# Kernel optimization log

Measured on AMD Instinct MI355X. Metric: run time of the kernel, lower is better.

Reference implementation:

```python
import jax, jax.numpy as jnp
import numpy as np

EPS = 1e-5  # torch LayerNorm default

def _layernorm(x, g, b):
    m = x.mean(-1, keepdims=True)
    v = ((x - m) ** 2).mean(-1, keepdims=True)
    return (x - m) * jax.lax.rsqrt(v + EPS) * g + b

def setup_inputs() -> dict:
    key = jax.random.key(0)
    ks = jax.random.split(key, 6)
    B, T, D, N, L = 16, 4096, 512, 77, 768
    s = 0.02
    return {
        "x": jax.random.normal(ks[0], (B, T, D), jnp.float32),
        "xf": jax.random.normal(ks[1], (B, N, L), jnp.float32),
        "q_w": jax.random.normal(ks[2], (D, D), jnp.float32) * s,
        "q_b": jnp.zeros((D,), jnp.float32),
        "k_w": jax.random.normal(ks[3], (D, L), jnp.float32) * s,
        "k_b": jnp.zeros((D,), jnp.float32),
        "v_w": jax.random.normal(ks[4], (D, L), jnp.float32) * s,
        "v_b": jnp.zeros((D,), jnp.float32),
        "norm_g": jnp.ones((D,), jnp.float32),
        "norm_b": jnp.zeros((D,), jnp.float32),
        "tnorm_g": jnp.ones((L,), jnp.float32),
        "tnorm_b": jnp.zeros((L,), jnp.float32),
        "num_heads": 8,
    }

def reference(x, xf, q_w, q_b, k_w, k_b, v_w, v_b, norm_g, norm_b, tnorm_g, tnorm_b, num_heads):
    B, T, D = x.shape
    N = xf.shape[1]
    H = num_heads
    xn = _layernorm(x, norm_g, norm_b)          # [B,T,D]
    xfn = _layernorm(xf, tnorm_g, tnorm_b)      # [B,N,L]
    # projections (torch Linear: y = x @ W^T + b)
    q = (xn @ q_w.T + q_b).reshape(B, T, H, -1)
    k = (xfn @ k_w.T + k_b).reshape(B, N, H, -1)
    v = (xfn @ v_w.T + v_b).reshape(B, N, H, -1)
    q = jax.nn.softmax(q, axis=-1)              # softmax over head feature dim
    k = jax.nn.softmax(k, axis=1)               # softmax over text token dim N
    # context: per-head [d,l] matrix, never materializes T x N scores
    att = jnp.einsum('bnhd,bnhl->bhdl', k, v)   # [B,H,d,l]
    y = jnp.einsum('bthd,bhdl->bthl', q, att).reshape(B, T, D)
    return x + y
```

## Files before the change

kernel.cpp:

```cpp
#include <hip/hip_runtime.h>

typedef __attribute__((ext_vector_type(8))) __bf16 bf16x8;
typedef __attribute__((ext_vector_type(4))) float f32x4;
typedef __attribute__((ext_vector_type(8))) unsigned short u16x8;
typedef __attribute__((ext_vector_type(4))) unsigned short u16x4;

#define MFMA16(a, b, c) __builtin_amdgcn_mfma_f32_16x16x32_bf16((a), (b), (c), 0, 0, 0)

static __device__ __forceinline__ unsigned short f2bf(float f) {
    union { float f; unsigned int u; } v;
    v.f = f;
    unsigned int r = v.u + 0x7FFFu + ((v.u >> 16) & 1u);
    return (unsigned short)(r >> 16);
}

__global__ __launch_bounds__(256) void prep_kernel(
    const float* __restrict__ qw, const float* __restrict__ kw,
    const float* __restrict__ vw,
    unsigned short* __restrict__ wfrag, unsigned short* __restrict__ kv_wf)
{
    const int idx = blockIdx.x * 256 + threadIdx.x;
    if (idx < 262144) {
        const int i = idx & 7, lane = (idx >> 3) & 63, kk = (idx >> 9) & 15, nb = idx >> 13;
        const int row = nb * 16 + (lane & 15);
        const int col = kk * 32 + ((lane >> 4) << 3) + i;
        wfrag[idx] = f2bf(qw[row * 512 + col]);
    } else {
        const int jdx = idx - 262144;
        const int i = jdx & 7, lane = (jdx >> 3) & 63;
        const int rest = jdx >> 9;
        const int kk = rest % 24, nb = rest / 24;
        const int j = nb * 16 + (lane & 15);
        const int k = kk * 32 + ((lane >> 4) << 3) + i;
        kv_wf[jdx] = f2bf(j < 512 ? kw[j * 768 + k] : vw[(j - 512) * 768 + k]);
    }
}

#define LDK 776
__global__ __launch_bounds__(256) void kv_kernel(
    const float* __restrict__ xf, const unsigned short* __restrict__ kv_wf,
    const float* __restrict__ kb, const float* __restrict__ vb,
    const float* __restrict__ tg, const float* __restrict__ tb,
    float* __restrict__ kv)
{
    __shared__ unsigned short xfn[80 * LDK];
    const int tid = threadIdx.x;
    const int lane = tid & 63;
    const int w = tid >> 6;
    const int l15 = lane & 15;
    const int lg = lane >> 4;
    const int b = blockIdx.y;
    const int jt = blockIdx.x;

    float g[12], be[12];
#pragma unroll
    for (int c = 0; c < 3; ++c) {
        const float4 gv = *(const float4*)(tg + c * 256 + lane * 4);
        const float4 bv = *(const float4*)(tb + c * 256 + lane * 4);
        g[c*4+0]=gv.x; g[c*4+1]=gv.y; g[c*4+2]=gv.z; g[c*4+3]=gv.w;
        be[c*4+0]=bv.x; be[c*4+1]=bv.y; be[c*4+2]=bv.z; be[c*4+3]=bv.w;
    }

    for (int n = w; n < 77; n += 4) {
        const float* xr = xf + (long)(b * 77 + n) * 768;
        float vals[12];
#pragma unroll
        for (int c = 0; c < 3; ++c) {
            const float4 v4 = *(const float4*)(xr + c * 256 + lane * 4);
            vals[c*4+0]=v4.x; vals[c*4+1]=v4.y; vals[c*4+2]=v4.z; vals[c*4+3]=v4.w;
        }
        float s = 0.f, ss = 0.f;
#pragma unroll
        for (int j = 0; j < 12; ++j) { s += vals[j]; ss += vals[j] * vals[j]; }
#pragma unroll
        for (int off = 32; off > 0; off >>= 1) {
            s += __shfl_xor(s, off);
            ss += __shfl_xor(ss, off);
        }
        const float mean = s * (1.f / 768.f);
        const float var = ss * (1.f / 768.f) - mean * mean;
        const float rstd = rsqrtf(var + 1e-5f);
#pragma unroll
        for (int c = 0; c < 3; ++c) {
            u16x4 o;
#pragma unroll
            for (int q = 0; q < 4; ++q)
                o[q] = f2bf((vals[c*4+q] - mean) * rstd * g[c*4+q] + be[c*4+q]);
            *(u16x4*)&xfn[n * LDK + c * 256 + lane * 4] = o;
        }
    }
    for (int idx = tid; idx < 3 * 768; idx += 256)
        xfn[(77 + idx / 768) * LDK + (idx % 768)] = 0;
    __syncthreads();

    const int nb = jt * 4 + w;
    f32x4 acc[5];
#pragma unroll
    for (int m = 0; m < 5; ++m) { acc[m][0]=0.f; acc[m][1]=0.f; acc[m][2]=0.f; acc[m][3]=0.f; }
    for (int kk = 0; kk < 24; ++kk) {
        const bf16x8 bw = *(const bf16x8*)&kv_wf[((nb * 24 + kk) * 64 + lane) * 8];
#pragma unroll
        for (int m = 0; m < 5; ++m) {
            const bf16x8 a = *(const bf16x8*)&xfn[(m * 16 + l15) * LDK + kk * 32 + lg * 8];
            acc[m] = MFMA16(a, bw, acc[m]);
        }
    }
    const int j = nb * 16 + l15;
    const float bias = (j < 512) ? kb[j] : vb[j - 512];
#pragma unroll
    for (int m = 0; m < 5; ++m) {
#pragma unroll
        for (int reg = 0; reg < 4; ++reg) {
            const int n = m * 16 + lg * 4 + reg;
            if (n < 77)
                kv[(long)(b * 77 + n) * 1024 + j] = acc[m][reg] + bias;
        }
    }
}

__global__ __launch_bounds__(256) void att_kernel(
    const float* __restrict__ kv, unsigned short* __restrict__ att_fr)
{
    const int b = blockIdx.x >> 3;
    const int h = blockIdx.x & 7;
    __shared__ float k_lds[77][65];
    __shared__ float v_lds[77][65];
    __shared__ float att_lds[64][65];
    const int tid = threadIdx.x;

    for (int idx = tid; idx < 77 * 64; idx += 256) {
        const int n = idx >> 6, d = idx & 63;
        const long base = (long)(b * 77 + n) * 1024 + h * 64 + d;
        k_lds[n][d] = kv[base];
        v_lds[n][d] = kv[base + 512];
    }
    __syncthreads();
    if (tid < 64) {
        float mx = -1e30f;
        for (int n = 0; n < 77; ++n) mx = fmaxf(mx, k_lds[n][tid]);
        float s = 0.f;
        for (int n = 0; n < 77; ++n) {
            const float e = __expf(k_lds[n][tid] - mx);
            k_lds[n][tid] = e;
            s += e;
        }
        const float inv = 1.f / s;
        for (int n = 0; n < 77; ++n) k_lds[n][tid] *= inv;
    }
    __syncthreads();
    {
        const int l = tid & 63, db = (tid >> 6) * 16;
        float a[16];
#pragma unroll
        for (int i = 0; i < 16; ++i) a[i] = 0.f;
        for (int n = 0; n < 77; ++n) {
            const float vv = v_lds[n][l];
#pragma unroll
            for (int i = 0; i < 16; ++i) a[i] += k_lds[n][db + i] * vv;
        }
#pragma unroll
        for (int i = 0; i < 16; ++i) att_lds[db + i][l] = a[i];
    }
    __syncthreads();
    const long hb8 = (long)(b * 8 + h) * 4096;
    for (int idx = tid; idx < 4096; idx += 256) {
        const int i = idx & 7, lane = (idx >> 3) & 63, kk = (idx >> 9) & 1, nf = (idx >> 10);
        const int d = kk * 32 + ((lane >> 4) << 3) + i;
        const int l = nf * 16 + (lane & 15);
        att_fr[hb8 + (long)(nf * 2 + kk) * 512 + lane * 8 + i] = f2bf(att_lds[d][l]);
    }
}

#define LDA 520
#define LDY 516

#define WLD(n, kk) (*(const bf16x8*)&wfrag[((((wc * 8 + (n)) * 16 + (kk)) * 64) + lane) * 8])
#define ALD(m, kk) (*(const bf16x8*)&xn[(wr * 32 + (m) * 16 + l15) * LDA + (kk) * 32 + lg * 8])

__global__ __launch_bounds__(512, 4) void fused3(
    const float* __restrict__ x, const unsigned short* __restrict__ wfrag,
    const float* __restrict__ qb, const float* __restrict__ ng,
    const float* __restrict__ nbt, const unsigned short* __restrict__ att_fr,
    float* __restrict__ out)
{
    __shared__ char smem[64 * LDA * 2];
    unsigned short* const xn = (unsigned short*)smem;
    float* const ylds = (float*)smem;
    const int tid = threadIdx.x;
    const int lane = tid & 63;
    const int w = tid >> 6;
    const int l15 = lane & 15;
    const int lg = lane >> 4;
    const int wr = w >> 2, wc = w & 3;
    const int b = blockIdx.y;
    const long rowbase = (long)b * 4096 + (long)blockIdx.x * 64;
    const float* xblk = x + rowbase * 512;

    float g[8], be[8];
    {
        const float4 g0 = *(const float4*)(ng + lane * 8);
        const float4 g1 = *(const float4*)(ng + lane * 8 + 4);
        const float4 b0 = *(const float4*)(nbt + lane * 8);
        const float4 b1 = *(const float4*)(nbt + lane * 8 + 4);
        g[0]=g0.x; g[1]=g0.y; g[2]=g0.z; g[3]=g0.w;
        g[4]=g1.x; g[5]=g1.y; g[6]=g1.z; g[7]=g1.w;
        be[0]=b0.x; be[1]=b0.y; be[2]=b0.z; be[3]=b0.w;
        be[4]=b1.x; be[5]=b1.y; be[6]=b1.z; be[7]=b1.w;
    }

    {
        float vals[8][8];
#pragma unroll
        for (int r = 0; r < 8; ++r) {
            const float* xr = xblk + (w * 8 + r) * 512 + lane * 8;
            const float4 v0 = *(const float4*)xr;
            const float4 v1 = *(const float4*)(xr + 4);
            vals[r][0]=v0.x; vals[r][1]=v0.y; vals[r][2]=v0.z; vals[r][3]=v0.w;
            vals[r][4]=v1.x; vals[r][5]=v1.y; vals[r][6]=v1.z; vals[r][7]=v1.w;
        }
#pragma unroll
        for (int r = 0; r < 8; ++r) {
            float s = 0.f, ss = 0.f;
#pragma unroll
            for (int j = 0; j < 8; ++j) { s += vals[r][j]; ss += vals[r][j] * vals[r][j]; }
#pragma unroll
            for (int off = 32; off > 0; off >>= 1) {
                s += __shfl_xor(s, off);
                ss += __shfl_xor(ss, off);
            }
            const float mean = s * (1.f / 512.f);
            const float var = ss * (1.f / 512.f) - mean * mean;
            const float rstd = rsqrtf(var + 1e-5f);
            u16x8 o;
#pragma unroll
            for (int j = 0; j < 8; ++j)
                o[j] = f2bf((vals[r][j] - mean) * rstd * g[j] + be[j]);
            *(u16x8*)&xn[(w * 8 + r) * LDA + lane * 8] = o;
        }
    }
    __syncthreads();

    const int wcol = wc * 128;
    f32x4 acc[2][8];
#pragma unroll
    for (int n = 0; n < 8; ++n) {
        const float qbv = qb[wcol + n * 16 + l15];
#pragma unroll
        for (int m = 0; m < 2; ++m) {
            acc[m][n][0]=qbv; acc[m][n][1]=qbv; acc[m][n][2]=qbv; acc[m][n][3]=qbv;
        }
    }

    bf16x8 aC0 = ALD(0, 0), aC1 = ALD(1, 0);
    bf16x8 bC0 = WLD(0, 0), bC1 = WLD(1, 0), bC2 = WLD(2, 0), bC3 = WLD(3, 0);
#pragma unroll
    for (int kk = 0; kk < 16; ++kk) {
        bf16x8 bN0 = WLD(4, kk), bN1 = WLD(5, kk), bN2 = WLD(6, kk), bN3 = WLD(7, kk);
        acc[0][0] = MFMA16(aC0, bC0, acc[0][0]); acc[1][0] = MFMA16(aC1, bC0, acc[1][0]);
        acc[0][1] = MFMA16(aC0, bC1, acc[0][1]); acc[1][1] = MFMA16(aC1, bC1, acc[1][1]);
        acc[0][2] = MFMA16(aC0, bC2, acc[0][2]); acc[1][2] = MFMA16(aC1, bC2, acc[1][2]);
        acc[0][3] = MFMA16(aC0, bC3, acc[0][3]); acc[1][3] = MFMA16(aC1, bC3, acc[1][3]);
        bf16x8 a2_0 = aC0, a2_1 = aC1;
        if (kk < 15) {
            a2_0 = ALD(0, kk + 1); a2_1 = ALD(1, kk + 1);
            bC0 = WLD(0, kk + 1); bC1 = WLD(1, kk + 1);
            bC2 = WLD(2, kk + 1); bC3 = WLD(3, kk + 1);
        }
        acc[0][4] = MFMA16(aC0, bN0, acc[0][4]); acc[1][4] = MFMA16(aC1, bN0, acc[1][4]);
        acc[0][5] = MFMA16(aC0, bN1, acc[0][5]); acc[1][5] = MFMA16(aC1, bN1, acc[1][5]);
        acc[0][6] = MFMA16(aC0, bN2, acc[0][6]); acc[1][6] = MFMA16(aC1, bN2, acc[1][6]);
        acc[0][7] = MFMA16(aC0, bN3, acc[0][7]); acc[1][7] = MFMA16(aC1, bN3, acc[1][7]);
        aC0 = a2_0; aC1 = a2_1;
    }

#pragma unroll
    for (int m = 0; m < 2; ++m) {
#pragma unroll
        for (int hb = 0; hb < 2; ++hb) {
#pragma unroll
            for (int reg = 0; reg < 4; ++reg) {
                float mx = fmaxf(fmaxf(acc[m][hb*4+0][reg], acc[m][hb*4+1][reg]),
                                 fmaxf(acc[m][hb*4+2][reg], acc[m][hb*4+3][reg]));
#pragma unroll
                for (int off = 1; off < 16; off <<= 1)
                    mx = fmaxf(mx, __shfl_xor(mx, off));
                const float e0 = __expf(acc[m][hb*4+0][reg] - mx);
                const float e1 = __expf(acc[m][hb*4+1][reg] - mx);
                const float e2 = __expf(acc[m][hb*4+2][reg] - mx);
                const float e3 = __expf(acc[m][hb*4+3][reg] - mx);
                float sm = e0 + e1 + e2 + e3;
#pragma unroll
                for (int off = 1; off < 16; off <<= 1)
                    sm += __shfl_xor(sm, off);
                const float inv = 1.f / sm;
                acc[m][hb*4+0][reg] = e0 * inv;
                acc[m][hb*4+1][reg] = e1 * inv;
                acc[m][hb*4+2][reg] = e2 * inv;
                acc[m][hb*4+3][reg] = e3 * inv;
            }
        }
    }

    const int h = w;
    const int colbase = h * 64;
    bf16x8 att_b[2][4];
#pragma unroll
    for (int kk = 0; kk < 2; ++kk)
#pragma unroll
        for (int nf = 0; nf < 4; ++nf)
            att_b[kk][nf] = *(const bf16x8*)&att_fr[
                (long)(b * 8 + h) * 4096 + (long)(nf * 2 + kk) * 512 + lane * 8];

    __syncthreads();
#pragma unroll
    for (int m = 0; m < 2; ++m)
#pragma unroll
        for (int n = 0; n < 8; ++n)
#pragma unroll
            for (int reg = 0; reg < 4; ++reg)
                xn[(wr * 32 + m * 16 + lg * 4 + reg) * LDA + wcol + n * 16 + l15] =
                    f2bf(acc[m][n][reg]);
    __syncthreads();

    f32x4 acc2[4][4];
#pragma unroll
    for (int m2 = 0; m2 < 4; ++m2)
#pragma unroll
        for (int nf = 0; nf < 4; ++nf) {
            acc2[m2][nf][0]=0.f; acc2[m2][nf][1]=0.f; acc2[m2][nf][2]=0.f; acc2[m2][nf][3]=0.f;
        }
#pragma unroll
    for (int kk = 0; kk < 2; ++kk) {
        bf16x8 a2[4];
#pragma unroll
        for (int m2 = 0; m2 < 4; ++m2)
            a2[m2] = *(const bf16x8*)&xn[(m2 * 16 + l15) * LDA + colbase + kk * 32 + lg * 8];
#pragma unroll
        for (int nf = 0; nf < 4; ++nf) {
#pragma unroll
            for (int m2 = 0; m2 < 4; ++m2)
                acc2[m2][nf] = MFMA16(a2[m2], att_b[kk][nf], acc2[m2][nf]);
        }
    }
    __syncthreads();

#pragma unroll
    for (int hh = 0; hh < 2; ++hh) {
#pragma unroll
        for (int m2h = 0; m2h < 2; ++m2h) {
            const int m2 = hh * 2 + m2h;
#pragma unroll
            for (int nf = 0; nf < 4; ++nf)
#pragma unroll
                for (int reg = 0; reg < 4; ++reg)
                    ylds[(m2h * 16 + lg * 4 + reg) * LDY + colbase + nf * 16 + l15] =
                        acc2[m2][nf][reg];
        }
        __syncthreads();
        const int row = tid >> 4;
        const long grow = rowbase + hh * 32 + row;
#pragma unroll
        for (int j = 0; j < 8; ++j) {
            const int col = j * 64 + (tid & 15) * 4;
            const float4 yv = *(const float4*)&ylds[row * LDY + col];
            const long gi = grow * 512 + col;
            const float4 xv = *(const float4*)&x[gi];
            float4 ov;
            ov.x = xv.x + yv.x; ov.y = xv.y + yv.y;
            ov.z = xv.z + yv.z; ov.w = xv.w + yv.w;
            *(float4*)&out[gi] = ov;
        }
        __syncthreads();
    }
}

extern "C" void kernel_launch(void* const* d_in, const int* in_sizes, int n_in,
                              void* d_out, int out_size, void* d_ws, size_t ws_size,
                              hipStream_t stream) {
    const float* x  = (const float*)d_in[0];
    const float* xf = (const float*)d_in[1];
    const float* qw = (const float*)d_in[2];
    const float* qb = (const float*)d_in[3];
    const float* kw = (const float*)d_in[4];
    const float* kb = (const float*)d_in[5];
    const float* vw = (const float*)d_in[6];
    const float* vb = (const float*)d_in[7];
    const float* ng = (const float*)d_in[8];
    const float* nb = (const float*)d_in[9];
    const float* tg = (const float*)d_in[10];
    const float* tb = (const float*)d_in[11];
    float* out = (float*)d_out;

    char* ws = (char*)d_ws;
    unsigned short* wfrag  = (unsigned short*)(ws);
    unsigned short* kv_wf  = (unsigned short*)(ws + 524288);
    float*          kv     = (float*)(ws + 2097152);
    unsigned short* att_fr = (unsigned short*)(ws + 7143424);

    prep_kernel<<<dim3(4096), dim3(256), 0, stream>>>(qw, kw, vw, wfrag, kv_wf);
    kv_kernel<<<dim3(16, 16), dim3(256), 0, stream>>>(xf, kv_wf, kb, vb, tg, tb, kv);
    att_kernel<<<dim3(128), dim3(256), 0, stream>>>(kv, att_fr);
    fused3<<<dim3(64, 16), dim3(512), 0, stream>>>(x, wfrag, qb, ng, nb, att_fr, out);
}
```

Before: 156.5 us.

## Assign each wave one head's full 64x64 Q tile to drop a barrier

The Q-projection GEMM is re-tiled so that each of the 8 waves computes all 64 rows for its own 64-column head slice, replacing the earlier 32x128 per-wave tile. The head-feature softmax and the following context matmul then stay within one wave. The barrier between writing bf16 Q to LDS and reading it back can be removed because each wave only reads the columns it wrote. The trade-off is that each wave now loads 4 A fragments and 4 B fragments per k-step instead of 2 and 8, and the per-step software prefetch pattern changes.

```diff
diff --git a/kernel.cpp b/kernel.cpp
--- a/kernel.cpp
+++ b/kernel.cpp
@@ -174,10 +174,10 @@
 #define LDA 520
 #define LDY 516
 
-#define WLD(n, kk) (*(const bf16x8*)&wfrag[((((wc * 8 + (n)) * 16 + (kk)) * 64) + lane) * 8])
-#define ALD(m, kk) (*(const bf16x8*)&xn[(wr * 32 + (m) * 16 + l15) * LDA + (kk) * 32 + lg * 8])
-
-__global__ __launch_bounds__(512, 4) void fused3(
+#define WLD(n, kk) (*(const bf16x8*)&wfrag[((((w * 4 + (n)) * 16 + (kk)) * 64) + lane) * 8])
+#define ALD(m, kk) (*(const bf16x8*)&xn[((m) * 16 + l15) * LDA + (kk) * 32 + lg * 8])
+
+__global__ __launch_bounds__(512, 4) void fused4(
     const float* __restrict__ x, const unsigned short* __restrict__ wfrag,
     const float* __restrict__ qb, const float* __restrict__ ng,
     const float* __restrict__ nbt, const unsigned short* __restrict__ att_fr,
@@ -191,7 +191,6 @@
     const int w = tid >> 6;
     const int l15 = lane & 15;
     const int lg = lane >> 4;
-    const int wr = w >> 2, wc = w & 3;
     const int b = blockIdx.y;
     const long rowbase = (long)b * 4096 + (long)blockIdx.x * 64;
     const float* xblk = x + rowbase * 512;
@@ -240,87 +239,89 @@
     }
     __syncthreads();
 
-    const int wcol = wc * 128;
-    f32x4 acc[2][8];
-#pragma unroll
-    for (int n = 0; n < 8; ++n) {
+    const int wcol = w * 64;
+    f32x4 acc[4][4];
+#pragma unroll
+    for (int n = 0; n < 4; ++n) {
         const float qbv = qb[wcol + n * 16 + l15];
 #pragma unroll
-        for (int m = 0; m < 2; ++m) {
+        for (int m = 0; m < 4; ++m) {
             acc[m][n][0]=qbv; acc[m][n][1]=qbv; acc[m][n][2]=qbv; acc[m][n][3]=qbv;
         }
     }
 
-    bf16x8 aC0 = ALD(0, 0), aC1 = ALD(1, 0);
-    bf16x8 bC0 = WLD(0, 0), bC1 = WLD(1, 0), bC2 = WLD(2, 0), bC3 = WLD(3, 0);
-#pragma unroll
-    for (int kk = 0; kk < 16; ++kk) {
-        bf16x8 bN0 = WLD(4, kk), bN1 = WLD(5, kk), bN2 = WLD(6, kk), bN3 = WLD(7, kk);
-        acc[0][0] = MFMA16(aC0, bC0, acc[0][0]); acc[1][0] = MFMA16(aC1, bC0, acc[1][0]);
-        acc[0][1] = MFMA16(aC0, bC1, acc[0][1]); acc[1][1] = MFMA16(aC1, bC1, acc[1][1]);
-        acc[0][2] = MFMA16(aC0, bC2, acc[0][2]); acc[1][2] = MFMA16(aC1, bC2, acc[1][2]);
-        acc[0][3] = MFMA16(aC0, bC3, acc[0][3]); acc[1][3] = MFMA16(aC1, bC3, acc[1][3]);
-        bf16x8 a2_0 = aC0, a2_1 = aC1;
-        if (kk < 15) {
-            a2_0 = ALD(0, kk + 1); a2_1 = ALD(1, kk + 1);
-            bC0 = WLD(0, kk + 1); bC1 = WLD(1, kk + 1);
-            bC2 = WLD(2, kk + 1); bC3 = WLD(3, kk + 1);
-        }
-        acc[0][4] = MFMA16(aC0, bN0, acc[0][4]); acc[1][4] = MFMA16(aC1, bN0, acc[1][4]);
-        acc[0][5] = MFMA16(aC0, bN1, acc[0][5]); acc[1][5] = MFMA16(aC1, bN1, acc[1][5]);
-        acc[0][6] = MFMA16(aC0, bN2, acc[0][6]); acc[1][6] = MFMA16(aC1, bN2, acc[1][6]);
-        acc[0][7] = MFMA16(aC0, bN3, acc[0][7]); acc[1][7] = MFMA16(aC1, bN3, acc[1][7]);
-        aC0 = a2_0; aC1 = a2_1;
-    }
-
-#pragma unroll
-    for (int m = 0; m < 2; ++m) {
-#pragma unroll
-        for (int hb = 0; hb < 2; ++hb) {
-#pragma unroll
-            for (int reg = 0; reg < 4; ++reg) {
-                float mx = fmaxf(fmaxf(acc[m][hb*4+0][reg], acc[m][hb*4+1][reg]),
-                                 fmaxf(acc[m][hb*4+2][reg], acc[m][hb*4+3][reg]));
-#pragma unroll
-                for (int off = 1; off < 16; off <<= 1)
-                    mx = fmaxf(mx, __shfl_xor(mx, off));
-                const float e0 = __expf(acc[m][hb*4+0][reg] - mx);
-                const float e1 = __expf(acc[m][hb*4+1][reg] - mx);
-                const float e2 = __expf(acc[m][hb*4+2][reg] - mx);
-                const float e3 = __expf(acc[m][hb*4+3][reg] - mx);
-                float sm = e0 + e1 + e2 + e3;
-#pragma unroll
-                for (int off = 1; off < 16; off <<= 1)
-                    sm += __shfl_xor(sm, off);
-                const float inv = 1.f / sm;
-                acc[m][hb*4+0][reg] = e0 * inv;
-                acc[m][hb*4+1][reg] = e1 * inv;
-                acc[m][hb*4+2][reg] = e2 * inv;
-                acc[m][hb*4+3][reg] = e3 * inv;
+    {
+        bf16x8 aC[4], bC[4];
+#pragma unroll
+        for (int m = 0; m < 4; ++m) aC[m] = ALD(m, 0);
+#pragma unroll
+        for (int n = 0; n < 4; ++n) bC[n] = WLD(n, 0);
+#pragma unroll
+        for (int kk = 0; kk < 16; ++kk) {
+            bf16x8 aN[4], bN[4];
+            if (kk < 15) {
+#pragma unroll
+                for (int m = 0; m < 4; ++m) aN[m] = ALD(m, kk + 1);
+#pragma unroll
+                for (int n = 0; n < 4; ++n) bN[n] = WLD(n, kk + 1);
             }
-        }
-    }
-
-    const int h = w;
-    const int colbase = h * 64;
+#pragma unroll
+            for (int n = 0; n < 4; ++n)
+#pragma unroll
+                for (int m = 0; m < 4; ++m)
+                    acc[m][n] = MFMA16(aC[m], bC[n], acc[m][n]);
+            if (kk < 15) {
+#pragma unroll
+                for (int m = 0; m < 4; ++m) aC[m] = aN[m];
+#pragma unroll
+                for (int n = 0; n < 4; ++n) bC[n] = bN[n];
+            }
+        }
+    }
+
+#pragma unroll
+    for (int m = 0; m < 4; ++m) {
+#pragma unroll
+        for (int reg = 0; reg < 4; ++reg) {
+            float mx = fmaxf(fmaxf(acc[m][0][reg], acc[m][1][reg]),
+                             fmaxf(acc[m][2][reg], acc[m][3][reg]));
+#pragma unroll
+            for (int off = 1; off < 16; off <<= 1)
+                mx = fmaxf(mx, __shfl_xor(mx, off));
+            const float e0 = __expf(acc[m][0][reg] - mx);
+            const float e1 = __expf(acc[m][1][reg] - mx);
+            const float e2 = __expf(acc[m][2][reg] - mx);
+            const float e3 = __expf(acc[m][3][reg] - mx);
+            float sm = e0 + e1 + e2 + e3;
+#pragma unroll
+            for (int off = 1; off < 16; off <<= 1)
+                sm += __shfl_xor(sm, off);
+            const float inv = 1.f / sm;
+            acc[m][0][reg] = e0 * inv;
+            acc[m][1][reg] = e1 * inv;
+            acc[m][2][reg] = e2 * inv;
+            acc[m][3][reg] = e3 * inv;
+        }
+    }
+
     bf16x8 att_b[2][4];
 #pragma unroll
     for (int kk = 0; kk < 2; ++kk)
 #pragma unroll
         for (int nf = 0; nf < 4; ++nf)
             att_b[kk][nf] = *(const bf16x8*)&att_fr[
-                (long)(b * 8 + h) * 4096 + (long)(nf * 2 + kk) * 512 + lane * 8];
-
-    __syncthreads();
-#pragma unroll
-    for (int m = 0; m < 2; ++m)
-#pragma unroll
-        for (int n = 0; n < 8; ++n)
+                (long)(b * 8 + w) * 4096 + (long)(nf * 2 + kk) * 512 + lane * 8];
+
+    __syncthreads();
+
+#pragma unroll
+    for (int m = 0; m < 4; ++m)
+#pragma unroll
+        for (int n = 0; n < 4; ++n)
 #pragma unroll
             for (int reg = 0; reg < 4; ++reg)
-                xn[(wr * 32 + m * 16 + lg * 4 + reg) * LDA + wcol + n * 16 + l15] =
+                xn[(m * 16 + lg * 4 + reg) * LDA + wcol + n * 16 + l15] =
                     f2bf(acc[m][n][reg]);
-    __syncthreads();
 
     f32x4 acc2[4][4];
 #pragma unroll
@@ -334,7 +335,7 @@
         bf16x8 a2[4];
 #pragma unroll
         for (int m2 = 0; m2 < 4; ++m2)
-            a2[m2] = *(const bf16x8*)&xn[(m2 * 16 + l15) * LDA + colbase + kk * 32 + lg * 8];
+            a2[m2] = *(const bf16x8*)&xn[(m2 * 16 + l15) * LDA + wcol + kk * 32 + lg * 8];
 #pragma unroll
         for (int nf = 0; nf < 4; ++nf) {
 #pragma unroll
@@ -353,7 +354,7 @@
             for (int nf = 0; nf < 4; ++nf)
 #pragma unroll
                 for (int reg = 0; reg < 4; ++reg)
-                    ylds[(m2h * 16 + lg * 4 + reg) * LDY + colbase + nf * 16 + l15] =
+                    ylds[(m2h * 16 + lg * 4 + reg) * LDY + wcol + nf * 16 + l15] =
                         acc2[m2][nf][reg];
         }
         __syncthreads();
@@ -400,5 +401,5 @@
     prep_kernel<<<dim3(4096), dim3(256), 0, stream>>>(qw, kw, vw, wfrag, kv_wf);
     kv_kernel<<<dim3(16, 16), dim3(256), 0, stream>>>(xf, kv_wf, kb, vb, tg, tb, kv);
     att_kernel<<<dim3(128), dim3(256), 0, stream>>>(kv, att_fr);
-    fused3<<<dim3(64, 16), dim3(512), 0, stream>>>(x, wfrag, qb, ng, nb, att_fr, out);
-}
+    fused4<<<dim3(64, 16), dim3(512), 0, stream>>>(x, wfrag, qb, ng, nb, att_fr, out);
+}
```

After: 144.9 us. 7.4% less time.
